# Kernel tuning notes

Hardware: AMD Instinct MI355X
Metric: run time of the kernel (lower is better)

The kernel has to match this reference:

```python
import jax, jax.numpy as jnp
import numpy as np

HEADS = 16
LN_EPS = 1e-5

def _ln(v, w, b):
    # LayerNorm over last dim (head dim s)
    mu = jnp.mean(v, axis=-1, keepdims=True)
    var = jnp.mean(jnp.square(v - mu), axis=-1, keepdims=True)
    return (v - mu) * jax.lax.rsqrt(var + LN_EPS) * w + b

def setup_inputs() -> dict:
    key = jax.random.key(0)
    ks = jax.random.split(key, 5)
    b, t, e = 2, 2048, 1024
    x = jax.random.normal(ks[0], (b, t, e), dtype=jnp.float32)
    scale = 0.02
    Wk = jax.random.normal(ks[1], (e, e), dtype=jnp.float32) * scale
    Wq = jax.random.normal(ks[2], (e, e), dtype=jnp.float32) * scale
    Wv = jax.random.normal(ks[3], (e, e), dtype=jnp.float32) * scale
    Wu = jax.random.normal(ks[4], (e, e), dtype=jnp.float32) * scale
    s = e // HEADS
    return {
        "x": x, "Wk": Wk, "Wq": Wq, "Wv": Wv, "Wu": Wu,
        "kln_w": jnp.ones((s,), jnp.float32), "kln_b": jnp.zeros((s,), jnp.float32),
        "qln_w": jnp.ones((s,), jnp.float32), "qln_b": jnp.zeros((s,), jnp.float32),
    }

def reference(x, Wk, Wq, Wv, Wu, kln_w, kln_b, qln_w, qln_b):
    b, t, e = x.shape
    h = HEADS
    s = e // h
    # nn.Linear: y = x @ W^T
    k = (x @ Wk.T).reshape(b, t, h, s)
    q = (x @ Wq.T).reshape(b, t, h, s)
    v = (x @ Wv.T).reshape(b, t, h, s)
    k = _ln(k, kln_w, kln_b)
    q = _ln(q, qln_w, qln_b)
    scalefactor = 1.0 / np.sqrt(s).astype(np.float32)
    # [b, h, t_q, t_k]
    dot = jnp.einsum('bqhs,bkhs->bhqk', q, k) * scalefactor
    causal = jnp.triu(jnp.ones((t, t), dtype=bool), k=1)  # mask strictly-upper (diag kept)
    dot = jnp.where(causal, -jnp.inf, dot)
    attn = jax.nn.softmax(dot, axis=-1)
    out = jnp.einsum('bhqk,bkhs->bqhs', attn, v).reshape(b, t, e)
    return out @ Wu.T
```

## Files before the change

### kernel.cpp

```cpp
#include <hip/hip_runtime.h>
#include <math.h>

#define T_SEQ 2048
#define E_DIM 1024
#define NH    16
#define HS    64
#define NB    2
#define M_ROWS 4096

typedef __attribute__((ext_vector_type(8))) short bf16x8;
typedef __attribute__((ext_vector_type(4))) short bf16x4;
typedef __attribute__((ext_vector_type(4))) float f32x4;

#define AS1 __attribute__((address_space(1)))
#define AS3 __attribute__((address_space(3)))

#define LOG2E 1.4426950408889634f

__device__ __forceinline__ f32x4 mfma16(bf16x4 a, bf16x4 b, f32x4 c) {
    return __builtin_amdgcn_mfma_f32_16x16x16bf16_1k(a, b, c, 0, 0, 0);
}

__device__ __forceinline__ ushort f2bf(float f) {
    union { float f; unsigned u; } c; c.f = f;
    unsigned r = c.u + 0x7fffu + ((c.u >> 16) & 1u);
    return (ushort)(r >> 16);
}
__device__ __forceinline__ ushort f2bf_trunc(float f) {
    union { float f; unsigned u; } c; c.f = f;
    return (ushort)(c.u >> 16);
}

__device__ __forceinline__ void load_lds16(const ushort* g, ushort* l) {
    __builtin_amdgcn_global_load_lds((const AS1 unsigned int*)g,
                                     (AS3 unsigned int*)l, 16, 0, 0);
}

__global__ __launch_bounds__(256) void cvt_all(
    const float* __restrict__ x,  const float* __restrict__ Wk,
    const float* __restrict__ Wq, const float* __restrict__ Wv,
    const float* __restrict__ Wu,
    ushort* __restrict__ xb,  ushort* __restrict__ Wkb,
    ushort* __restrict__ Wqb, ushort* __restrict__ Wvb,
    ushort* __restrict__ Wub)
{
    int i4 = blockIdx.x * 256 + threadIdx.x;
    int region = i4 >> 18;
    const float* src; ushort* dst; int off;
    if      (region < 4)  { src = x;  dst = xb;  off = i4; }
    else if (region == 4) { src = Wk; dst = Wkb; off = i4 - (4 << 18); }
    else if (region == 5) { src = Wq; dst = Wqb; off = i4 - (5 << 18); }
    else if (region == 6) { src = Wv; dst = Wvb; off = i4 - (6 << 18); }
    else                  { src = Wu; dst = Wub; off = i4 - (7 << 18); }
    float4 v = *(const float4*)(src + (size_t)off * 4);
    ushort4 o; o.x = f2bf(v.x); o.y = f2bf(v.y); o.z = f2bf(v.z); o.w = f2bf(v.w);
    *(ushort4*)(dst + (size_t)off * 4) = o;
}

__device__ __forceinline__ void gemm_core_db(
    const ushort* __restrict__ A, const ushort* __restrict__ W,
    int m0, int n0, ushort* As, ushort* Bs, f32x4 acc[4][4])
{
    const int tid  = threadIdx.x;
    const int lane = tid & 63, w = tid >> 6;
    const int quad = lane >> 4, l16 = lane & 15;
    const int wm = w & 1, wn = w >> 1;

    const int rl   = lane >> 2;
    const int gsw  = (lane & 3) ^ ((lane >> 3) & 3);
    const int fsw  = (l16 >> 1) & 3;

    const f32x4 zero = {0.f, 0.f, 0.f, 0.f};
#pragma unroll
    for (int mt = 0; mt < 4; ++mt)
#pragma unroll
        for (int nt = 0; nt < 4; ++nt) acc[mt][nt] = zero;

#pragma unroll
    for (int i = 0; i < 2; ++i) {
        int c = i * 4 + w;
        int row = c * 16 + rl;
        load_lds16(A + (size_t)(m0 + row) * E_DIM + gsw * 8, As + c * 512);
        load_lds16(W + (size_t)(n0 + row) * E_DIM + gsw * 8, Bs + c * 512);
    }

    for (int k0 = 0; k0 < E_DIM; k0 += 32) {
        const int buf = (k0 >> 5) & 1;
        ushort* Ab = As + buf * 4096;
        ushort* Bb = Bs + buf * 4096;
        __syncthreads();
        if (k0 + 32 < E_DIM) {
            ushort* An = As + (buf ^ 1) * 4096;
            ushort* Bn = Bs + (buf ^ 1) * 4096;
#pragma unroll
            for (int i = 0; i < 2; ++i) {
                int c = i * 4 + w;
                int row = c * 16 + rl;
                load_lds16(A + (size_t)(m0 + row) * E_DIM + k0 + 32 + gsw * 8,
                           An + c * 512);
                load_lds16(W + (size_t)(n0 + row) * E_DIM + k0 + 32 + gsw * 8,
                           Bn + c * 512);
            }
        }
        bf16x8 af[4], bfr[4];
#pragma unroll
        for (int mt = 0; mt < 4; ++mt)
            af[mt] = *(const bf16x8*)(Ab + (wm * 64 + mt * 16 + l16) * 32
                                      + ((quad ^ fsw) * 8));
#pragma unroll
        for (int nt = 0; nt < 4; ++nt)
            bfr[nt] = *(const bf16x8*)(Bb + (wn * 64 + nt * 16 + l16) * 32
                                       + ((quad ^ fsw) * 8));
#pragma unroll
        for (int mt = 0; mt < 4; ++mt)
#pragma unroll
            for (int nt = 0; nt < 4; ++nt)
                acc[mt][nt] = __builtin_amdgcn_mfma_f32_16x16x32_bf16(
                    af[mt], bfr[nt], acc[mt][nt], 0, 0, 0);
    }
}

__global__ __launch_bounds__(256) void gemm_qkv(
    const ushort* __restrict__ A,
    const ushort* __restrict__ W0, const ushort* __restrict__ W1,
    const ushort* __restrict__ W2,
    ushort* __restrict__ Kb, ushort* __restrict__ Qb, ushort* __restrict__ Vt,
    const float* __restrict__ kw, const float* __restrict__ kbias,
    const float* __restrict__ qw, const float* __restrict__ qbias)
{
    __shared__ ushort As[2 * 128 * 32];
    __shared__ ushort Bs[2 * 128 * 32];
    const int z = blockIdx.z;
    const ushort* W = (z == 0) ? W0 : (z == 1) ? W1 : W2;
    const int m0 = blockIdx.y * 128, n0 = blockIdx.x * 128;
    f32x4 acc[4][4];
    gemm_core_db(A, W, m0, n0, As, Bs, acc);

    const int lane = threadIdx.x & 63, w = threadIdx.x >> 6;
    const int quad = lane >> 4, l16 = lane & 15;
    const int wm = w & 1, wn = w >> 1;
    const int row0 = m0 + wm * 64;
    const int col0 = n0 + wn * 64;

    if (z < 2) {
        ushort* C = z ? Qb : Kb;
        const float* lw = z ? qw : kw;
        const float* lb = z ? qbias : kbias;
        const float scale = z ? (0.125f * LOG2E) : 1.0f;
        float wv[4], bv_[4];
#pragma unroll
        for (int nt = 0; nt < 4; ++nt) {
            wv[nt]  = lw[nt * 16 + l16];
            bv_[nt] = lb[nt * 16 + l16];
        }
#pragma unroll
        for (int mt = 0; mt < 4; ++mt)
#pragma unroll
            for (int r = 0; r < 4; ++r) {
                float v[4], d[4];
#pragma unroll
                for (int nt = 0; nt < 4; ++nt) v[nt] = acc[mt][nt][r];
                float s = v[0] + v[1] + v[2] + v[3];
                s += __shfl_xor(s, 1); s += __shfl_xor(s, 2);
                s += __shfl_xor(s, 4); s += __shfl_xor(s, 8);
                float mu = s * (1.0f / 64.0f);
                float q2 = 0.f;
#pragma unroll
                for (int nt = 0; nt < 4; ++nt) { d[nt] = v[nt] - mu; q2 += d[nt] * d[nt]; }
                q2 += __shfl_xor(q2, 1); q2 += __shfl_xor(q2, 2);
                q2 += __shfl_xor(q2, 4); q2 += __shfl_xor(q2, 8);
                float rin = rsqrtf(q2 * (1.0f / 64.0f) + 1e-5f);
                int row = row0 + mt * 16 + quad * 4 + r;
#pragma unroll
                for (int nt = 0; nt < 4; ++nt)
                    C[(size_t)row * E_DIM + col0 + nt * 16 + l16] =
                        f2bf((d[nt] * rin * wv[nt] + bv_[nt]) * scale);
            }
    } else {
        const int bidx = m0 >> 11;
        const int hh   = col0 >> 6;
        const int t0   = (m0 & 2047) + wm * 64;
#pragma unroll
        for (int mt = 0; mt < 4; ++mt)
#pragma unroll
            for (int nt = 0; nt < 4; ++nt) {
                ushort4 pk = make_ushort4(f2bf(acc[mt][nt][0]), f2bf(acc[mt][nt][1]),
                                          f2bf(acc[mt][nt][2]), f2bf(acc[mt][nt][3]));
                size_t off = ((size_t)(bidx * NH + hh) * 64 + nt * 16 + l16) * T_SEQ
                             + t0 + mt * 16 + quad * 4;
                *(ushort4*)(Vt + off) = pk;
            }
    }
}

__global__ __launch_bounds__(256) void gemm_o(
    const ushort* __restrict__ A, const ushort* __restrict__ W,
    float* __restrict__ C)
{
    __shared__ ushort As[2 * 128 * 32];
    __shared__ ushort Bs[2 * 128 * 32];
    const int m0 = blockIdx.y * 128, n0 = blockIdx.x * 128;
    f32x4 acc[4][4];
    gemm_core_db(A, W, m0, n0, As, Bs, acc);

    const int lane = threadIdx.x & 63, w = threadIdx.x >> 6;
    const int quad = lane >> 4, l16 = lane & 15;
    const int row0 = m0 + (w & 1) * 64;
    const int col0 = n0 + (w >> 1) * 64;
#pragma unroll
    for (int mt = 0; mt < 4; ++mt)
#pragma unroll
        for (int nt = 0; nt < 4; ++nt)
#pragma unroll
            for (int r = 0; r < 4; ++r)
                C[(size_t)(row0 + mt * 16 + quad * 4 + r) * E_DIM
                  + col0 + nt * 16 + l16] = acc[mt][nt][r];
}

__global__ __launch_bounds__(256, 5) void flash_attn6(
    const ushort* __restrict__ Qg, const ushort* __restrict__ Kg,
    const ushort* __restrict__ Vt, float* __restrict__ Pbuf,
    float* __restrict__ Lbuf)
{
    __shared__ ushort Ks[2][64 * 64];
    __shared__ ushort Vs[2][64 * 64];

    const int tid  = threadIdx.x;
    const int lane = tid & 63, w = tid >> 6;
    const int quad = lane >> 4, l16 = lane & 15;

    const int pair  = blockIdx.x >> 1;
    const int split = blockIdx.x & 1;
    const int bh = pair & 31;
    const int qt = 31 - (pair >> 5);
    const int b = bh >> 4, h = bh & 15;

    const int ntile = qt + 1;
    const int hmid  = ntile >> 1;
    const int jt0 = split ? hmid  : 0;
    const int jt1 = split ? ntile : hmid;
    if (jt0 >= jt1) return;

    const int slot = (bh << 5) | qt;

    const ushort* Qbase = Qg + ((size_t)b * T_SEQ) * E_DIM + h * HS;
    const ushort* Kbase = Kg + ((size_t)b * T_SEQ) * E_DIM + h * HS;
    const ushort* Vbase = Vt + ((size_t)bh * HS) * T_SEQ;

    const int rloc = lane >> 3;
    const int gswc = (lane & 7) ^ rloc;
    const int sw   = l16 & 7;

    bf16x8 aq[2];
#pragma unroll
    for (int ks = 0; ks < 2; ++ks)
        aq[ks] = *(const bf16x8*)(Qbase + (size_t)(qt * 64 + w * 16 + l16) * E_DIM
                                  + ks * 32 + quad * 8);

    const f32x4 zero = {0.f, 0.f, 0.f, 0.f};
    f32x4 o_acc[4];
#pragma unroll
    for (int dt = 0; dt < 4; ++dt) o_acc[dt] = zero;
    float l_acc = 0.f;

#pragma unroll
    for (int i = 0; i < 2; ++i) {
        int cc = w * 2 + i, row = cc * 8 + rloc;
        load_lds16(Kbase + (size_t)(jt0 * 64 + row) * E_DIM + gswc * 8,
                   Ks[0] + cc * 512);
        load_lds16(Vbase + (size_t)row * T_SEQ + jt0 * 64 + gswc * 8,
                   Vs[0] + cc * 512);
    }

    const float M8 = 8.0f * LOG2E;

    for (int jt = jt0; jt < jt1; ++jt) {
        const int buf = (jt - jt0) & 1;
        __syncthreads();
        if (jt + 1 < jt1) {
#pragma unroll
            for (int i = 0; i < 2; ++i) {
                int cc = w * 2 + i, row = cc * 8 + rloc;
                load_lds16(Kbase + (size_t)(jt + 1) * 64 * E_DIM
                           + (size_t)row * E_DIM + gswc * 8, Ks[buf ^ 1] + cc * 512);
                load_lds16(Vbase + (size_t)row * T_SEQ + (jt + 1) * 64 + gswc * 8,
                           Vs[buf ^ 1] + cc * 512);
            }
        }

        f32x4 sa[4];
#pragma unroll
        for (int nt = 0; nt < 4; ++nt) sa[nt] = zero;
        __builtin_amdgcn_s_setprio(1);
#pragma unroll
        for (int ks = 0; ks < 2; ++ks) {
            int cp = ((ks * 4 + quad) ^ sw) * 8;
#pragma unroll
            for (int nt = 0; nt < 4; ++nt) {
                bf16x8 bk = *(const bf16x8*)(Ks[buf] + (nt * 16 + l16) * 64 + cp);
                sa[nt] = __builtin_amdgcn_mfma_f32_16x16x32_bf16(bk, aq[ks], sa[nt], 0, 0, 0);
            }
        }
        __builtin_amdgcn_s_setprio(0);

        if (jt == qt) {
#pragma unroll
            for (int nt = 0; nt < 4; ++nt)
#pragma unroll
                for (int r = 0; r < 4; ++r)
                    if (nt * 16 + quad * 4 + r > w * 16 + l16) sa[nt][r] = -1e30f;
        }

        bf16x4 bp[4];
        float lp[4];
#pragma unroll
        for (int nt = 0; nt < 4; ++nt) {
            float p0 = __builtin_amdgcn_exp2f(sa[nt][0] - M8);
            float p1 = __builtin_amdgcn_exp2f(sa[nt][1] - M8);
            float p2 = __builtin_amdgcn_exp2f(sa[nt][2] - M8);
            float p3 = __builtin_amdgcn_exp2f(sa[nt][3] - M8);
            bp[nt][0] = (short)f2bf_trunc(p0);
            bp[nt][1] = (short)f2bf_trunc(p1);
            bp[nt][2] = (short)f2bf_trunc(p2);
            bp[nt][3] = (short)f2bf_trunc(p3);
            lp[nt] = (p0 + p1) + (p2 + p3);
        }
        l_acc += (lp[0] + lp[1]) + (lp[2] + lp[3]);

        __builtin_amdgcn_s_setprio(1);
#pragma unroll
        for (int kt = 0; kt < 4; ++kt) {
            const int tt = kt * 16 + quad * 4;
            const int ch = tt >> 3, el = tt & 7;
#pragma unroll
            for (int dt = 0; dt < 4; ++dt) {
                const int vd = dt * 16 + l16;
                bf16x4 va = *(const bf16x4*)(Vs[buf] + vd * 64
                                             + ((ch ^ (vd & 7)) << 3) + el);
                o_acc[dt] = mfma16(va, bp[kt], o_acc[dt]);
            }
        }
        __builtin_amdgcn_s_setprio(0);
    }

    l_acc += __shfl_xor(l_acc, 16);
    l_acc += __shfl_xor(l_acc, 32);
    float* Po = Pbuf + (((size_t)split << 22) | ((size_t)slot << 12));
    const int q = w * 16 + l16;
#pragma unroll
    for (int dt = 0; dt < 4; ++dt)
        *(f32x4*)(Po + q * 64 + dt * 16 + quad * 4) = o_acc[dt];
    if (quad == 0) Lbuf[(split << 16) | (slot << 6) | q] = l_acc;
}

__global__ __launch_bounds__(256) void attn_merge(
    const float* __restrict__ Pbuf, const float* __restrict__ Lbuf,
    ushort* __restrict__ O)
{
    const int slot = blockIdx.x;
    const int bh = slot >> 5, qt = slot & 31;
    const int b = bh >> 4, h = bh & 15;
    const int tid = threadIdx.x;
    const int dl = (tid & 15) * 4;
    const int qh = tid >> 4;
    const bool has0 = (qt > 0);
    const float* P0 = Pbuf + ((size_t)slot << 12);
    const float* P1 = P0 + ((size_t)1 << 22);
#pragma unroll
    for (int j = 0; j < 4; ++j) {
        const int q = j * 16 + qh;
        float l = Lbuf[(1 << 16) | (slot << 6) | q];
        if (has0) l += Lbuf[(slot << 6) | q];
        const float inv = 1.0f / l;
        float4 c = *(const float4*)(P1 + q * 64 + dl);
        if (has0) {
            float4 a = *(const float4*)(P0 + q * 64 + dl);
            c.x += a.x; c.y += a.y; c.z += a.z; c.w += a.w;
        }
        ushort4 pk = make_ushort4(f2bf(c.x * inv), f2bf(c.y * inv),
                                  f2bf(c.z * inv), f2bf(c.w * inv));
        *(ushort4*)(O + ((size_t)(b * T_SEQ + qt * 64 + q)) * E_DIM
                    + h * HS + dl) = pk;
    }
}

extern "C" void kernel_launch(void* const* d_in, const int* in_sizes, int n_in,
                              void* d_out, int out_size, void* d_ws, size_t ws_size,
                              hipStream_t stream) {
    const float* x     = (const float*)d_in[0];
    const float* Wk    = (const float*)d_in[1];
    const float* Wq    = (const float*)d_in[2];
    const float* Wv    = (const float*)d_in[3];
    const float* Wu    = (const float*)d_in[4];
    const float* kln_w = (const float*)d_in[5];
    const float* kln_b = (const float*)d_in[6];
    const float* qln_w = (const float*)d_in[7];
    const float* qln_b = (const float*)d_in[8];
    float* out = (float*)d_out;

    const size_t NE = (size_t)M_ROWS * E_DIM;
    const size_t NW = (size_t)E_DIM * E_DIM;
    ushort* xb  = (ushort*)d_ws;
    ushort* Wkb = xb  + NE;
    ushort* Wqb = Wkb + NW;
    ushort* Wvb = Wqb + NW;
    ushort* Wub = Wvb + NW;
    ushort* Kb  = Wub + NW;
    ushort* Qb  = Kb  + NE;
    ushort* Vt  = Qb  + NE;
    ushort* Ob  = Vt  + NE;
    float*  Pbuf = (float*)(Ob + NE);
    float*  Lbuf = Pbuf + ((size_t)2 << 22);

    cvt_all<<<8192, 256, 0, stream>>>(x, Wk, Wq, Wv, Wu, xb, Wkb, Wqb, Wvb, Wub);

    gemm_qkv<<<dim3(E_DIM / 128, M_ROWS / 128, 3), 256, 0, stream>>>(
        xb, Wkb, Wqb, Wvb, Kb, Qb, Vt, kln_w, kln_b, qln_w, qln_b);

    flash_attn6<<<2048, 256, 0, stream>>>(Qb, Kb, Vt, Pbuf, Lbuf);
    attn_merge<<<1024, 256, 0, stream>>>(Pbuf, Lbuf, Ob);

    gemm_o<<<dim3(E_DIM / 128, M_ROWS / 128), 256, 0, stream>>>(Ob, Wub, out);
}
```

Before: 185.4 us.

## Use 256x256 triple-buffered GEMM tiles with swizzled block order for QKV and output

Both projection GEMMs move from 128x128 double-buffered tiles with 256 threads to 256x256 tiles with 512 threads and a three-stage LDS pipeline. The pipeline uses explicit vmcnt waits and raised wave priority around the MFMA block. QKV becomes one fused launch over the contiguous Wk/Wq/Wv buffer, and a swizzled block index groups tiles for L2 reuse. The aim is higher arithmetic intensity per LDS load and better latency hiding. The cost is fewer blocks (192 and 64), which may underfill the 256 CUs, plus more registers and 96KB of LDS per block.

Result: slower. 196.5 us (+6.0%).

```diff
diff --git a/kernel.cpp b/kernel.cpp
--- a/kernel.cpp
+++ b/kernel.cpp
@@ -57,9 +57,9 @@
     *(ushort4*)(dst + (size_t)off * 4) = o;
 }
 
-__device__ __forceinline__ void gemm_core_db(
+__device__ __forceinline__ void gemm_core_tb(
     const ushort* __restrict__ A, const ushort* __restrict__ W,
-    int m0, int n0, ushort* As, ushort* Bs, f32x4 acc[4][4])
+    int m0, int n0, ushort* smem, f32x4 acc[8][4])
 {
     const int tid  = threadIdx.x;
     const int lane = tid & 63, w = tid >> 6;
@@ -70,77 +70,88 @@
     const int gsw  = (lane & 3) ^ ((lane >> 3) & 3);
     const int fsw  = (l16 >> 1) & 3;
 
+    ushort* SA = smem;
+    ushort* SB = smem + 3 * 8192;
+
     const f32x4 zero = {0.f, 0.f, 0.f, 0.f};
 #pragma unroll
-    for (int mt = 0; mt < 4; ++mt)
+    for (int mt = 0; mt < 8; ++mt)
 #pragma unroll
         for (int nt = 0; nt < 4; ++nt) acc[mt][nt] = zero;
 
-#pragma unroll
-    for (int i = 0; i < 2; ++i) {
-        int c = i * 4 + w;
-        int row = c * 16 + rl;
-        load_lds16(A + (size_t)(m0 + row) * E_DIM + gsw * 8, As + c * 512);
-        load_lds16(W + (size_t)(n0 + row) * E_DIM + gsw * 8, Bs + c * 512);
-    }
-
-    for (int k0 = 0; k0 < E_DIM; k0 += 32) {
-        const int buf = (k0 >> 5) & 1;
-        ushort* Ab = As + buf * 4096;
-        ushort* Bb = Bs + buf * 4096;
-        __syncthreads();
-        if (k0 + 32 < E_DIM) {
-            ushort* An = As + (buf ^ 1) * 4096;
-            ushort* Bn = Bs + (buf ^ 1) * 4096;
-#pragma unroll
-            for (int i = 0; i < 2; ++i) {
-                int c = i * 4 + w;
-                int row = c * 16 + rl;
-                load_lds16(A + (size_t)(m0 + row) * E_DIM + k0 + 32 + gsw * 8,
-                           An + c * 512);
-                load_lds16(W + (size_t)(n0 + row) * E_DIM + k0 + 32 + gsw * 8,
-                           Bn + c * 512);
-            }
-        }
-        bf16x8 af[4], bfr[4];
-#pragma unroll
-        for (int mt = 0; mt < 4; ++mt)
-            af[mt] = *(const bf16x8*)(Ab + (wm * 64 + mt * 16 + l16) * 32
+    const ushort* Ag = A + (size_t)(m0 + rl) * E_DIM + gsw * 8;
+    const ushort* Bg = W + (size_t)(n0 + rl) * E_DIM + gsw * 8;
+
+#define STAGE_TB(j, tt) do {                                                  \
+        const int k0_ = (tt) * 32;                                            \
+        _Pragma("unroll")                                                     \
+        for (int i_ = 0; i_ < 2; ++i_) {                                      \
+            const int c_ = i_ * 8 + w;                                        \
+            load_lds16(Ag + (size_t)(c_ * 16) * E_DIM + k0_,                  \
+                       SA + (j) * 8192 + c_ * 512);                           \
+            load_lds16(Bg + (size_t)(c_ * 16) * E_DIM + k0_,                  \
+                       SB + (j) * 8192 + c_ * 512);                           \
+        } } while (0)
+
+    STAGE_TB(0, 0);
+    STAGE_TB(1, 1);
+
+    for (int t = 0; t < 32; ++t) {
+        if (t < 31) asm volatile("s_waitcnt vmcnt(4)" ::: "memory");
+        else        asm volatile("s_waitcnt vmcnt(0)" ::: "memory");
+        __builtin_amdgcn_s_barrier();
+        if (t + 2 < 32) {
+            const int j2 = (t + 2) % 3;
+            STAGE_TB(j2, t + 2);
+        }
+        const int cur = t % 3;
+        const ushort* Ab = SA + cur * 8192;
+        const ushort* Bb = SB + cur * 8192;
+        bf16x8 af[8], bfr[4];
+#pragma unroll
+        for (int mt = 0; mt < 8; ++mt)
+            af[mt] = *(const bf16x8*)(Ab + (wm * 128 + mt * 16 + l16) * 32
                                       + ((quad ^ fsw) * 8));
 #pragma unroll
         for (int nt = 0; nt < 4; ++nt)
             bfr[nt] = *(const bf16x8*)(Bb + (wn * 64 + nt * 16 + l16) * 32
                                        + ((quad ^ fsw) * 8));
-#pragma unroll
-        for (int mt = 0; mt < 4; ++mt)
+        __builtin_amdgcn_s_setprio(1);
+#pragma unroll
+        for (int mt = 0; mt < 8; ++mt)
 #pragma unroll
             for (int nt = 0; nt < 4; ++nt)
                 acc[mt][nt] = __builtin_amdgcn_mfma_f32_16x16x32_bf16(
                     af[mt], bfr[nt], acc[mt][nt], 0, 0, 0);
-    }
-}
-
-__global__ __launch_bounds__(256) void gemm_qkv(
-    const ushort* __restrict__ A,
-    const ushort* __restrict__ W0, const ushort* __restrict__ W1,
-    const ushort* __restrict__ W2,
+        __builtin_amdgcn_s_setprio(0);
+    }
+#undef STAGE_TB
+}
+
+__global__ __launch_bounds__(512, 2) void gemm_qkv_tb(
+    const ushort* __restrict__ A, const ushort* __restrict__ Wqkv,
     ushort* __restrict__ Kb, ushort* __restrict__ Qb, ushort* __restrict__ Vt,
     const float* __restrict__ kw, const float* __restrict__ kbias,
     const float* __restrict__ qw, const float* __restrict__ qbias)
 {
-    __shared__ ushort As[2 * 128 * 32];
-    __shared__ ushort Bs[2 * 128 * 32];
-    const int z = blockIdx.z;
-    const ushort* W = (z == 0) ? W0 : (z == 1) ? W1 : W2;
-    const int m0 = blockIdx.y * 128, n0 = blockIdx.x * 128;
-    f32x4 acc[4][4];
-    gemm_core_db(A, W, m0, n0, As, Bs, acc);
+    extern __shared__ ushort smem[];
+
+    const int lid = blockIdx.x;
+    const int swz = (lid & 7) * 24 + (lid >> 3);
+    const int m0  = (swz & 15) * 256;
+    const int n0  = (swz >> 4) * 256;
+
+    f32x4 acc[8][4];
+    gemm_core_tb(A, Wqkv, m0, n0, smem, acc);
 
     const int lane = threadIdx.x & 63, w = threadIdx.x >> 6;
     const int quad = lane >> 4, l16 = lane & 15;
     const int wm = w & 1, wn = w >> 1;
-    const int row0 = m0 + wm * 64;
-    const int col0 = n0 + wn * 64;
+
+    const int z    = n0 >> 10;
+    const int ncol = n0 & 1023;
+    const int col0 = ncol + wn * 64;
+    const int row0 = m0 + wm * 128;
 
     if (z < 2) {
         ushort* C = z ? Qb : Kb;
@@ -154,7 +165,7 @@
             bv_[nt] = lb[nt * 16 + l16];
         }
 #pragma unroll
-        for (int mt = 0; mt < 4; ++mt)
+        for (int mt = 0; mt < 8; ++mt)
 #pragma unroll
             for (int r = 0; r < 4; ++r) {
                 float v[4], d[4];
@@ -179,9 +190,9 @@
     } else {
         const int bidx = m0 >> 11;
         const int hh   = col0 >> 6;
-        const int t0   = (m0 & 2047) + wm * 64;
-#pragma unroll
-        for (int mt = 0; mt < 4; ++mt)
+        const int t0   = (m0 & 2047) + wm * 128;
+#pragma unroll
+        for (int mt = 0; mt < 8; ++mt)
 #pragma unroll
             for (int nt = 0; nt < 4; ++nt) {
                 ushort4 pk = make_ushort4(f2bf(acc[mt][nt][0]), f2bf(acc[mt][nt][1]),
@@ -193,22 +204,26 @@
     }
 }
 
-__global__ __launch_bounds__(256) void gemm_o(
+__global__ __launch_bounds__(512, 2) void gemm_o_tb(
     const ushort* __restrict__ A, const ushort* __restrict__ W,
     float* __restrict__ C)
 {
-    __shared__ ushort As[2 * 128 * 32];
-    __shared__ ushort Bs[2 * 128 * 32];
-    const int m0 = blockIdx.y * 128, n0 = blockIdx.x * 128;
-    f32x4 acc[4][4];
-    gemm_core_db(A, W, m0, n0, As, Bs, acc);
+    extern __shared__ ushort smem[];
+
+    const int lid = blockIdx.x;
+    const int swz = (lid & 7) * 8 + (lid >> 3);
+    const int m0  = (swz & 15) * 256;
+    const int n0  = (swz >> 4) * 256;
+
+    f32x4 acc[8][4];
+    gemm_core_tb(A, W, m0, n0, smem, acc);
 
     const int lane = threadIdx.x & 63, w = threadIdx.x >> 6;
     const int quad = lane >> 4, l16 = lane & 15;
-    const int row0 = m0 + (w & 1) * 64;
+    const int row0 = m0 + (w & 1) * 128;
     const int col0 = n0 + (w >> 1) * 64;
 #pragma unroll
-    for (int mt = 0; mt < 4; ++mt)
+    for (int mt = 0; mt < 8; ++mt)
 #pragma unroll
         for (int nt = 0; nt < 4; ++nt)
 #pragma unroll
@@ -412,13 +427,22 @@
     float*  Pbuf = (float*)(Ob + NE);
     float*  Lbuf = Pbuf + ((size_t)2 << 22);
 
+    static int attr_done = 0;
+    if (!attr_done) {
+        hipFuncSetAttribute(reinterpret_cast<const void*>(gemm_qkv_tb),
+                            hipFuncAttributeMaxDynamicSharedMemorySize, 98304);
+        hipFuncSetAttribute(reinterpret_cast<const void*>(gemm_o_tb),
+                            hipFuncAttributeMaxDynamicSharedMemorySize, 98304);
+        attr_done = 1;
+    }
+
     cvt_all<<<8192, 256, 0, stream>>>(x, Wk, Wq, Wv, Wu, xb, Wkb, Wqb, Wvb, Wub);
 
-    gemm_qkv<<<dim3(E_DIM / 128, M_ROWS / 128, 3), 256, 0, stream>>>(
-        xb, Wkb, Wqb, Wvb, Kb, Qb, Vt, kln_w, kln_b, qln_w, qln_b);
+    gemm_qkv_tb<<<192, 512, 98304, stream>>>(
+        xb, Wkb, Kb, Qb, Vt, kln_w, kln_b, qln_w, qln_b);
 
     flash_attn6<<<2048, 256, 0, stream>>>(Qb, Kb, Vt, Pbuf, Lbuf);
     attn_merge<<<1024, 256, 0, stream>>>(Pbuf, Lbuf, Ob);
 
-    gemm_o<<<dim3(E_DIM / 128, M_ROWS / 128), 256, 0, stream>>>(Ob, Wub, out);
-}
+    gemm_o_tb<<<64, 512, 98304, stream>>>(Ob, Wub, out);
+}
```

## Fuse split-KV merge into flash attention via atomic last-block counter

Applied to the files above, without the earlier changes.

Removes the separate attn_merge kernel. Each split block writes its partial output and normalizer, then bumps a per-slot atomic counter, and the second block to finish merges both partials and writes the bf16 output. Slots with a single tile write the output directly. The counters are zeroed inside the conversion kernel. This saves one kernel launch and a full read pass over the partial buffer, at the cost of fences, an atomic and an extra barrier at the end of every attention block.

Measured after the change: 451.7 us. +143.6%, slower.

```diff
diff --git a/kernel.cpp b/kernel.cpp
--- a/kernel.cpp
+++ b/kernel.cpp
@@ -42,8 +42,12 @@
     const float* __restrict__ Wu,
     ushort* __restrict__ xb,  ushort* __restrict__ Wkb,
     ushort* __restrict__ Wqb, ushort* __restrict__ Wvb,
-    ushort* __restrict__ Wub)
+    ushort* __restrict__ Wub, int* __restrict__ Cnt)
 {
+    if (blockIdx.x == 0) {
+#pragma unroll
+        for (int i = 0; i < 4; ++i) Cnt[threadIdx.x * 4 + i] = 0;
+    }
     int i4 = blockIdx.x * 256 + threadIdx.x;
     int region = i4 >> 18;
     const float* src; ushort* dst; int off;
@@ -217,10 +221,10 @@
                   + col0 + nt * 16 + l16] = acc[mt][nt][r];
 }
 
-__global__ __launch_bounds__(256, 5) void flash_attn6(
+__global__ __launch_bounds__(256, 5) void flash_attn7(
     const ushort* __restrict__ Qg, const ushort* __restrict__ Kg,
     const ushort* __restrict__ Vt, float* __restrict__ Pbuf,
-    float* __restrict__ Lbuf)
+    float* __restrict__ Lbuf, ushort* __restrict__ O, int* __restrict__ Cnt)
 {
     __shared__ ushort Ks[2][64 * 64];
     __shared__ ushort Vs[2][64 * 64];
@@ -345,42 +349,49 @@
 
     l_acc += __shfl_xor(l_acc, 16);
     l_acc += __shfl_xor(l_acc, 32);
+    const int q = w * 16 + l16;
+    const int trow = qt * 64 + q;
+
+    if (hmid == 0) {
+        const float inv = 1.0f / l_acc;
+#pragma unroll
+        for (int dt = 0; dt < 4; ++dt) {
+            ushort4 pk = make_ushort4(f2bf(o_acc[dt][0] * inv), f2bf(o_acc[dt][1] * inv),
+                                      f2bf(o_acc[dt][2] * inv), f2bf(o_acc[dt][3] * inv));
+            *(ushort4*)(O + ((size_t)b * T_SEQ + trow) * E_DIM + h * HS
+                        + dt * 16 + quad * 4) = pk;
+        }
+        return;
+    }
+
     float* Po = Pbuf + (((size_t)split << 22) | ((size_t)slot << 12));
-    const int q = w * 16 + l16;
 #pragma unroll
     for (int dt = 0; dt < 4; ++dt)
         *(f32x4*)(Po + q * 64 + dt * 16 + quad * 4) = o_acc[dt];
     if (quad == 0) Lbuf[(split << 16) | (slot << 6) | q] = l_acc;
-}
-
-__global__ __launch_bounds__(256) void attn_merge(
-    const float* __restrict__ Pbuf, const float* __restrict__ Lbuf,
-    ushort* __restrict__ O)
-{
-    const int slot = blockIdx.x;
-    const int bh = slot >> 5, qt = slot & 31;
-    const int b = bh >> 4, h = bh & 15;
-    const int tid = threadIdx.x;
-    const int dl = (tid & 15) * 4;
-    const int qh = tid >> 4;
-    const bool has0 = (qt > 0);
-    const float* P0 = Pbuf + ((size_t)slot << 12);
-    const float* P1 = P0 + ((size_t)1 << 22);
-#pragma unroll
-    for (int j = 0; j < 4; ++j) {
-        const int q = j * 16 + qh;
-        float l = Lbuf[(1 << 16) | (slot << 6) | q];
-        if (has0) l += Lbuf[(slot << 6) | q];
-        const float inv = 1.0f / l;
-        float4 c = *(const float4*)(P1 + q * 64 + dl);
-        if (has0) {
-            float4 a = *(const float4*)(P0 + q * 64 + dl);
-            c.x += a.x; c.y += a.y; c.z += a.z; c.w += a.w;
-        }
-        ushort4 pk = make_ushort4(f2bf(c.x * inv), f2bf(c.y * inv),
-                                  f2bf(c.z * inv), f2bf(c.w * inv));
-        *(ushort4*)(O + ((size_t)(b * T_SEQ + qt * 64 + q)) * E_DIM
-                    + h * HS + dl) = pk;
+
+    __syncthreads();
+    volatile int* flag = (volatile int*)&Ks[0][0];
+    if (tid == 0) {
+        __threadfence();
+        *flag = (atomicAdd(&Cnt[slot], 1) == 1);
+    }
+    __syncthreads();
+    if (*flag) {
+        __threadfence();
+        const float* Pp = Pbuf + (((size_t)(split ^ 1) << 22) | ((size_t)slot << 12));
+        const float lp = Lbuf[((split ^ 1) << 16) | (slot << 6) | q];
+        const float inv = 1.0f / (l_acc + lp);
+#pragma unroll
+        for (int dt = 0; dt < 4; ++dt) {
+            f32x4 pv = *(const f32x4*)(Pp + q * 64 + dt * 16 + quad * 4);
+            ushort4 pk = make_ushort4(f2bf((o_acc[dt][0] + pv[0]) * inv),
+                                      f2bf((o_acc[dt][1] + pv[1]) * inv),
+                                      f2bf((o_acc[dt][2] + pv[2]) * inv),
+                                      f2bf((o_acc[dt][3] + pv[3]) * inv));
+            *(ushort4*)(O + ((size_t)b * T_SEQ + trow) * E_DIM + h * HS
+                        + dt * 16 + quad * 4) = pk;
+        }
     }
 }
 
@@ -411,14 +422,14 @@
     ushort* Ob  = Vt  + NE;
     float*  Pbuf = (float*)(Ob + NE);
     float*  Lbuf = Pbuf + ((size_t)2 << 22);
-
-    cvt_all<<<8192, 256, 0, stream>>>(x, Wk, Wq, Wv, Wu, xb, Wkb, Wqb, Wvb, Wub);
+    int*    Cnt  = (int*)(Lbuf + 2 * 65536);
+
+    cvt_all<<<8192, 256, 0, stream>>>(x, Wk, Wq, Wv, Wu, xb, Wkb, Wqb, Wvb, Wub, Cnt);
 
     gemm_qkv<<<dim3(E_DIM / 128, M_ROWS / 128, 3), 256, 0, stream>>>(
         xb, Wkb, Wqb, Wvb, Kb, Qb, Vt, kln_w, kln_b, qln_w, qln_b);
 
-    flash_attn6<<<2048, 256, 0, stream>>>(Qb, Kb, Vt, Pbuf, Lbuf);
-    attn_merge<<<1024, 256, 0, stream>>>(Pbuf, Lbuf, Ob);
+    flash_attn7<<<2048, 256, 0, stream>>>(Qb, Kb, Vt, Pbuf, Lbuf, Ob, Cnt);
 
     gemm_o<<<dim3(E_DIM / 128, M_ROWS / 128), 256, 0, stream>>>(Ob, Wub, out);
 }
```

## Fuse split-attention merge into output projection GEMM A-operand load

Applied to the files above, without the earlier changes.

Removes the separate attn_merge kernel and the bf16 O buffer. The output GEMM now reads both split partial accumulators and the L sums directly, normalizes them, converts to bf16 and writes the A tile into LDS with register prefetch of the next k-slab. This saves one launch and a full write and read of O. The cost is that each of the 8 column blocks re-reads the fp32 partials (about 4x the bytes of bf16 O, read 8 times), which adds global traffic and register pressure inside the GEMM main loop.

New measurement: 210.6 us. +13.6%, slower.

```diff
diff --git a/kernel.cpp b/kernel.cpp
--- a/kernel.cpp
+++ b/kernel.cpp
@@ -193,30 +193,6 @@
     }
 }
 
-__global__ __launch_bounds__(256) void gemm_o(
-    const ushort* __restrict__ A, const ushort* __restrict__ W,
-    float* __restrict__ C)
-{
-    __shared__ ushort As[2 * 128 * 32];
-    __shared__ ushort Bs[2 * 128 * 32];
-    const int m0 = blockIdx.y * 128, n0 = blockIdx.x * 128;
-    f32x4 acc[4][4];
-    gemm_core_db(A, W, m0, n0, As, Bs, acc);
-
-    const int lane = threadIdx.x & 63, w = threadIdx.x >> 6;
-    const int quad = lane >> 4, l16 = lane & 15;
-    const int row0 = m0 + (w & 1) * 64;
-    const int col0 = n0 + (w >> 1) * 64;
-#pragma unroll
-    for (int mt = 0; mt < 4; ++mt)
-#pragma unroll
-        for (int nt = 0; nt < 4; ++nt)
-#pragma unroll
-            for (int r = 0; r < 4; ++r)
-                C[(size_t)(row0 + mt * 16 + quad * 4 + r) * E_DIM
-                  + col0 + nt * 16 + l16] = acc[mt][nt][r];
-}
-
 __global__ __launch_bounds__(256, 5) void flash_attn6(
     const ushort* __restrict__ Qg, const ushort* __restrict__ Kg,
     const ushort* __restrict__ Vt, float* __restrict__ Pbuf,
@@ -353,35 +329,126 @@
     if (quad == 0) Lbuf[(split << 16) | (slot << 6) | q] = l_acc;
 }
 
-__global__ __launch_bounds__(256) void attn_merge(
+__global__ __launch_bounds__(256) void gemm_o_m(
     const float* __restrict__ Pbuf, const float* __restrict__ Lbuf,
-    ushort* __restrict__ O)
+    const ushort* __restrict__ W, float* __restrict__ C)
 {
-    const int slot = blockIdx.x;
-    const int bh = slot >> 5, qt = slot & 31;
-    const int b = bh >> 4, h = bh & 15;
-    const int tid = threadIdx.x;
-    const int dl = (tid & 15) * 4;
-    const int qh = tid >> 4;
-    const bool has0 = (qt > 0);
-    const float* P0 = Pbuf + ((size_t)slot << 12);
-    const float* P1 = P0 + ((size_t)1 << 22);
-#pragma unroll
-    for (int j = 0; j < 4; ++j) {
-        const int q = j * 16 + qh;
-        float l = Lbuf[(1 << 16) | (slot << 6) | q];
-        if (has0) l += Lbuf[(slot << 6) | q];
-        const float inv = 1.0f / l;
-        float4 c = *(const float4*)(P1 + q * 64 + dl);
-        if (has0) {
-            float4 a = *(const float4*)(P0 + q * 64 + dl);
-            c.x += a.x; c.y += a.y; c.z += a.z; c.w += a.w;
-        }
-        ushort4 pk = make_ushort4(f2bf(c.x * inv), f2bf(c.y * inv),
-                                  f2bf(c.z * inv), f2bf(c.w * inv));
-        *(ushort4*)(O + ((size_t)(b * T_SEQ + qt * 64 + q)) * E_DIM
-                    + h * HS + dl) = pk;
-    }
+    __shared__ ushort As[2 * 128 * 32];
+    __shared__ ushort Bs[2 * 128 * 32];
+
+    const int tid  = threadIdx.x;
+    const int lane = tid & 63, w = tid >> 6;
+    const int quad = lane >> 4, l16 = lane & 15;
+    const int wm = w & 1, wn = w >> 1;
+    const int m0 = blockIdx.y * 128, n0 = blockIdx.x * 128;
+
+    const int rl   = lane >> 2;
+    const int gsw  = (lane & 3) ^ ((lane >> 3) & 3);
+    const int fsw  = (l16 >> 1) & 3;
+
+    int  qv[2], sb[2];
+    bool h0[2];
+#pragma unroll
+    for (int ci = 0; ci < 2; ++ci) {
+        const int token = m0 + (ci * 4 + w) * 16 + rl;
+        const int qt = (token >> 6) & 31;
+        qv[ci] = token & 63;
+        sb[ci] = ((token >> 11) << 9) | qt;
+        h0[ci] = (qt > 0);
+    }
+
+    f32x4 p0a[2], p0b[2], p1a[2], p1b[2];
+    float l0v[2], l1v[2];
+
+#define ISSUE_A(k0_) do {                                                     \
+        const int e_  = (k0_) + gsw * 8;                                      \
+        const int h_  = e_ >> 6, d0_ = e_ & 63;                               \
+        _Pragma("unroll")                                                     \
+        for (int ci = 0; ci < 2; ++ci) {                                      \
+            const int slot_ = sb[ci] + (h_ << 5);                             \
+            const float* p0_ = Pbuf + ((size_t)slot_ << 12) + qv[ci] * 64 + d0_; \
+            const float* p1_ = p0_ + ((size_t)1 << 22);                       \
+            p0a[ci] = *(const f32x4*)p0_;  p0b[ci] = *(const f32x4*)(p0_ + 4);\
+            p1a[ci] = *(const f32x4*)p1_;  p1b[ci] = *(const f32x4*)(p1_ + 4);\
+            l0v[ci] = Lbuf[(slot_ << 6) | qv[ci]];                            \
+            l1v[ci] = Lbuf[(1 << 16) | (slot_ << 6) | qv[ci]];                \
+        } } while (0)
+
+#define WRITE_A(buf_) do {                                                    \
+        _Pragma("unroll")                                                     \
+        for (int ci = 0; ci < 2; ++ci) {                                      \
+            const int c_ = ci * 4 + w;                                        \
+            const float inv_ = 1.0f / (l1v[ci] + (h0[ci] ? l0v[ci] : 0.f));   \
+            bf16x8 vo;                                                        \
+            _Pragma("unroll")                                                 \
+            for (int j = 0; j < 4; ++j) {                                     \
+                float a0 = p1a[ci][j] + (h0[ci] ? p0a[ci][j] : 0.f);          \
+                float a1 = p1b[ci][j] + (h0[ci] ? p0b[ci][j] : 0.f);          \
+                vo[j]     = (short)f2bf(a0 * inv_);                           \
+                vo[4 + j] = (short)f2bf(a1 * inv_);                           \
+            }                                                                 \
+            *(bf16x8*)(As + (buf_) * 4096 + c_ * 512 + lane * 8) = vo;        \
+        } } while (0)
+
+    const f32x4 zero = {0.f, 0.f, 0.f, 0.f};
+    f32x4 acc[4][4];
+#pragma unroll
+    for (int mt = 0; mt < 4; ++mt)
+#pragma unroll
+        for (int nt = 0; nt < 4; ++nt) acc[mt][nt] = zero;
+
+    ISSUE_A(0);
+#pragma unroll
+    for (int i = 0; i < 2; ++i) {
+        int c = i * 4 + w, row = c * 16 + rl;
+        load_lds16(W + (size_t)(n0 + row) * E_DIM + gsw * 8, Bs + c * 512);
+    }
+    WRITE_A(0);
+
+    for (int k0 = 0; k0 < E_DIM; k0 += 32) {
+        const int buf = (k0 >> 5) & 1;
+        const ushort* Ab = As + buf * 4096;
+        const ushort* Bb = Bs + buf * 4096;
+        __syncthreads();
+        if (k0 + 32 < E_DIM) {
+            ISSUE_A(k0 + 32);
+#pragma unroll
+            for (int i = 0; i < 2; ++i) {
+                int c = i * 4 + w, row = c * 16 + rl;
+                load_lds16(W + (size_t)(n0 + row) * E_DIM + k0 + 32 + gsw * 8,
+                           Bs + (buf ^ 1) * 4096 + c * 512);
+            }
+        }
+        bf16x8 af[4], bfr[4];
+#pragma unroll
+        for (int mt = 0; mt < 4; ++mt)
+            af[mt] = *(const bf16x8*)(Ab + (wm * 64 + mt * 16 + l16) * 32
+                                      + ((quad ^ fsw) * 8));
+#pragma unroll
+        for (int nt = 0; nt < 4; ++nt)
+            bfr[nt] = *(const bf16x8*)(Bb + (wn * 64 + nt * 16 + l16) * 32
+                                       + ((quad ^ fsw) * 8));
+#pragma unroll
+        for (int mt = 0; mt < 4; ++mt)
+#pragma unroll
+            for (int nt = 0; nt < 4; ++nt)
+                acc[mt][nt] = __builtin_amdgcn_mfma_f32_16x16x32_bf16(
+                    af[mt], bfr[nt], acc[mt][nt], 0, 0, 0);
+        if (k0 + 32 < E_DIM) WRITE_A(buf ^ 1);
+    }
+#undef ISSUE_A
+#undef WRITE_A
+
+    const int row0 = m0 + wm * 64;
+    const int col0 = n0 + wn * 64;
+#pragma unroll
+    for (int mt = 0; mt < 4; ++mt)
+#pragma unroll
+        for (int nt = 0; nt < 4; ++nt)
+#pragma unroll
+            for (int r = 0; r < 4; ++r)
+                C[(size_t)(row0 + mt * 16 + quad * 4 + r) * E_DIM
+                  + col0 + nt * 16 + l16] = acc[mt][nt][r];
 }
 
 extern "C" void kernel_launch(void* const* d_in, const int* in_sizes, int n_in,
@@ -408,8 +475,7 @@
     ushort* Kb  = Wub + NW;
     ushort* Qb  = Kb  + NE;
     ushort* Vt  = Qb  + NE;
-    ushort* Ob  = Vt  + NE;
-    float*  Pbuf = (float*)(Ob + NE);
+    float*  Pbuf = (float*)(Vt + NE);
     float*  Lbuf = Pbuf + ((size_t)2 << 22);
 
     cvt_all<<<8192, 256, 0, stream>>>(x, Wk, Wq, Wv, Wu, xb, Wkb, Wqb, Wvb, Wub);
@@ -418,7 +484,7 @@
         xb, Wkb, Wqb, Wvb, Kb, Qb, Vt, kln_w, kln_b, qln_w, qln_b);
 
     flash_attn6<<<2048, 256, 0, stream>>>(Qb, Kb, Vt, Pbuf, Lbuf);
-    attn_merge<<<1024, 256, 0, stream>>>(Pbuf, Lbuf, Ob);
-
-    gemm_o<<<dim3(E_DIM / 128, M_ROWS / 128), 256, 0, stream>>>(Ob, Wub, out);
-}
+
+    gemm_o_m<<<dim3(E_DIM / 128, M_ROWS / 128), 256, 0, stream>>>(
+        Pbuf, Lbuf, Wub, out);
+}
```
